# Kernel tuning notes

Hardware: AMD Instinct MI355X
Metric: run time of the kernel (lower is better)

Reference implementation:

```python
import jax, jax.numpy as jnp
import numpy as np

CUTOFF = 3  # cutoff_freq default in low_pass_filter


def _low_pass(x):
    # full 2D FFT over (H, W), keep only the 4 corner blocks of size CUTOFF
    H, W = x.shape[-2], x.shape[-1]
    f = jnp.fft.fftn(x, axes=(-2, -1))
    mask = jnp.zeros((H, W), dtype=x.dtype)
    c = CUTOFF
    mask = mask.at[:c, :c].set(1).at[:c, -c:].set(1).at[-c:, :c].set(1).at[-c:, -c:].set(1)
    return jnp.abs(jnp.fft.ifftn(f * mask, axes=(-2, -1)))


def setup_inputs() -> dict:
    key = jax.random.key(0)
    k_x, k_w1, k_b1, k_w2, k_b2 = jax.random.split(key, 5)
    n_feat = 8
    B, C, H, W = 32, 3, 512, 512
    x = jax.random.uniform(k_x, (B, C, H, W), dtype=jnp.float32)
    # 1x1 convs == channel-mixing matrices; kaiming-ish scale
    w1 = jax.random.normal(k_w1, (n_feat, C), dtype=jnp.float32) * (1.0 / np.sqrt(C))
    b1 = jax.random.normal(k_b1, (n_feat,), dtype=jnp.float32) * 0.01
    w2 = jax.random.normal(k_w2, (C, n_feat), dtype=jnp.float32) * (1.0 / np.sqrt(n_feat))
    b2 = jax.random.normal(k_b2, (C,), dtype=jnp.float32) * 0.01
    return {"x": x, "w1": w1, "b1": b1, "w2": w2, "b2": b2}


def reference(x, w1, b1, w2, b2):
    lp = _low_pass(x)                                        # [B,3,H,W]
    h = jax.nn.relu(jnp.einsum('bchw,fc->bfhw', lp, w1) + b1[None, :, None, None])
    y = jnp.einsum('bfhw,cf->bchw', h, w2) + b2[None, :, None, None]
    return jnp.clip(y + lp, 0.0, 1.0)
```

## Files before the change

kernel.cpp:

```cpp
#include <hip/hip_runtime.h>
#include <math.h>


#define WS_TS 0
#define WS_F  6144
#define WS_A  12288
constexpr int NPART = 8;

__global__ __launch_bounds__(512, 6) void k_colsum(const float* __restrict__ x,
                                                   float* __restrict__ ws) {
    __shared__ float buf[3][128][29];
    float* A = ws + WS_A;
    int img = blockIdx.x >> 3;
    int slab = blockIdx.x & 7;
    int t = threadIdx.x;
    int wq = t & 127;
    int q = t >> 7;
    int h0 = slab * 64 + q * 16;
    const float* xp = x + (size_t)img * 262144 + (size_t)h0 * 512 + wq * 4;

    const float TH = 6.28318530717958647692f / 512.0f;
    float pc1, ps1, pc2, ps2, pc3, ps3;
    sincosf(TH * (float)h0, &ps1, &pc1);
    pc2 = pc1 * pc1 - ps1 * ps1;  ps2 = 2.f * pc1 * ps1;
    pc3 = pc1 * pc2 - ps1 * ps2;  ps3 = ps1 * pc2 + pc1 * ps2;
    const float C1 = 0.99992470183914450299f, S1 = 0.01227153828571992539f;
    const float C2 = 0.99969881869620422012f, S2 = 0.02454122852291228803f;
    const float C3 = 0.99932238458834954375f, S3 = 0.03680722294135883171f;

    float s0[4] = {0,0,0,0};
    float ar1[4] = {0,0,0,0}, ai1[4] = {0,0,0,0};
    float ar2[4] = {0,0,0,0}, ai2[4] = {0,0,0,0};
    float ar3[4] = {0,0,0,0}, ai3[4] = {0,0,0,0};

    float4 cur[4], nxt[4];
#pragma unroll
    for (int j = 0; j < 4; ++j) cur[j] = *(const float4*)(xp + (size_t)j * 512);
#pragma unroll
    for (int g = 0; g < 4; ++g) {
        if (g < 3) {
#pragma unroll
            for (int j = 0; j < 4; ++j)
                nxt[j] = *(const float4*)(xp + (size_t)((g + 1) * 4 + j) * 512);
        }
#pragma unroll
        for (int j = 0; j < 4; ++j) {
            float xa[4] = {cur[j].x, cur[j].y, cur[j].z, cur[j].w};
#pragma unroll
            for (int u = 0; u < 4; ++u) {
                s0[u] += xa[u];
                ar1[u] = fmaf(xa[u], pc1, ar1[u]);  ai1[u] = fmaf(-xa[u], ps1, ai1[u]);
                ar2[u] = fmaf(xa[u], pc2, ar2[u]);  ai2[u] = fmaf(-xa[u], ps2, ai2[u]);
                ar3[u] = fmaf(xa[u], pc3, ar3[u]);  ai3[u] = fmaf(-xa[u], ps3, ai3[u]);
            }
            float n;
            n = pc1 * C1 - ps1 * S1;  ps1 = ps1 * C1 + pc1 * S1;  pc1 = n;
            n = pc2 * C2 - ps2 * S2;  ps2 = ps2 * C2 + pc2 * S2;  pc2 = n;
            n = pc3 * C3 - ps3 * S3;  ps3 = ps3 * C3 + pc3 * S3;  pc3 = n;
        }
#pragma unroll
        for (int j = 0; j < 4; ++j) cur[j] = nxt[j];
    }

    if (q != 0) {
        float* r = &buf[q - 1][wq][0];
#pragma unroll
        for (int u = 0; u < 4; ++u) {
            r[u]      = s0[u];
            r[4 + u]  = ar1[u];  r[8 + u]  = ai1[u];
            r[12 + u] = ar2[u];  r[16 + u] = ai2[u];
            r[20 + u] = ar3[u];  r[24 + u] = ai3[u];
        }
    }
    __syncthreads();
    if (q == 0) {
#pragma unroll
        for (int v = 0; v < 3; ++v) {
            const float* r = &buf[v][wq][0];
#pragma unroll
            for (int u = 0; u < 4; ++u) {
                s0[u]  += r[u];
                ar1[u] += r[4 + u];   ai1[u] += r[8 + u];
                ar2[u] += r[12 + u];  ai2[u] += r[16 + u];
                ar3[u] += r[20 + u];  ai3[u] += r[24 + u];
            }
        }
        float* Ab = A + (((size_t)img * NPART + slab) * 8) * 512 + wq * 4;
        *(float4*)(Ab + 0 * 512) = make_float4(s0[0], s0[1], s0[2], s0[3]);
        *(float4*)(Ab + 1 * 512) = make_float4(0.f, 0.f, 0.f, 0.f);
        *(float4*)(Ab + 2 * 512) = make_float4(ar1[0], ar1[1], ar1[2], ar1[3]);
        *(float4*)(Ab + 3 * 512) = make_float4(ai1[0], ai1[1], ai1[2], ai1[3]);
        *(float4*)(Ab + 4 * 512) = make_float4(ar2[0], ar2[1], ar2[2], ar2[3]);
        *(float4*)(Ab + 5 * 512) = make_float4(ai2[0], ai2[1], ai2[2], ai2[3]);
        *(float4*)(Ab + 6 * 512) = make_float4(ar3[0], ar3[1], ar3[2], ar3[3]);
        *(float4*)(Ab + 7 * 512) = make_float4(ai3[0], ai3[1], ai3[2], ai3[3]);
    }
}

__global__ __launch_bounds__(256) void k_proj(float* __restrict__ ws) {
    int t = threadIdx.x;
    if (blockIdx.x == 96) {
        const float STEP = 6.28318530717958647692f / 512.0f;
        const int mv[6] = {0, 1, 2, -3, -2, -1};
        for (int h = t; h < 512; h += 256) {
            float* tsp = ws + WS_TS + h * 12;
#pragma unroll
            for (int i = 0; i < 6; ++i) {
                int r = ((mv[i] * h) % 512 + 512) & 511;
                float s, c;
                sincosf(STEP * (float)r, &s, &c);
                tsp[2 * i] = c; tsp[2 * i + 1] = s;
            }
        }
        return;
    }
    __shared__ float As[8][8][68];
    __shared__ float Rs[28][8][2];
    const float* A = ws + WS_A;
    float* F = ws + WS_F;
    int img = blockIdx.x;

    {
        int plane = t >> 5;
        int w0 = (t & 31) * 16;
        float4 acc[4];
#pragma unroll
        for (int u = 0; u < 4; ++u) acc[u] = make_float4(0.f, 0.f, 0.f, 0.f);
        const float* base = A + ((size_t)img * NPART * 8 + plane) * 512 + w0;
        for (int hg = 0; hg < NPART; ++hg) {
            const float* p = base + (size_t)hg * 8 * 512;
#pragma unroll
            for (int u = 0; u < 4; ++u) {
                float4 v = *(const float4*)(p + u * 4);
                acc[u].x += v.x; acc[u].y += v.y; acc[u].z += v.z; acc[u].w += v.w;
            }
        }
        int seg = w0 >> 6, j0 = w0 & 63;
#pragma unroll
        for (int u = 0; u < 4; ++u)
            *(float4*)&As[plane][seg][j0 + u * 4] = acc[u];
    }
    __syncthreads();

    if (t < 224) {
        int pair = t >> 3, seg = t & 7;
        int k = pair / 7, mi = pair % 7;
        float m = (float)(mi - 3);
        const float TH = 6.28318530717958647692f / 512.0f;
        float cm, sm, pc, ps;
        sincosf(-m * TH, &sm, &cm);
        sincosf(-m * TH * (float)(seg * 64), &ps, &pc);
        const float* Ar_ = &As[2 * k][seg][0];
        const float* Ai_ = &As[2 * k + 1][seg][0];
        float pre = 0.f, pim = 0.f;
#pragma unroll 4
        for (int j = 0; j < 64; ++j) {
            float Ar = Ar_[j], Ai = Ai_[j];
            pre += Ar * pc - Ai * ps;
            pim += Ar * ps + Ai * pc;
            float n = pc * cm - ps * sm;
            ps = ps * cm + pc * sm;
            pc = n;
        }
        Rs[pair][seg][0] = pre;
        Rs[pair][seg][1] = pim;
    }
    __syncthreads();
    if (t < 56) {
        int pair = t >> 1, part = t & 1;
        float s = 0.f;
#pragma unroll
        for (int g = 0; g < 8; ++g) s += Rs[pair][g][part];
        F[(size_t)img * 56 + t] = s;
    }
}

__global__ __launch_bounds__(256) void k_out(const float* __restrict__ ws,
                                             const float* __restrict__ w1,
                                             const float* __restrict__ b1,
                                             const float* __restrict__ w2,
                                             const float* __restrict__ b2,
                                             float* __restrict__ out) {
    const float* tabS = ws + WS_TS;
    const float* Fb = ws + WS_F;
    __shared__ float F_lds[3][56];
    __shared__ float T[4][3][12];
    int t = threadIdx.x;
    int blk = blockIdx.x;
    int b = blk >> 7;
    int h0 = (blk & 127) << 2;

    if (t < 168) {
        int c = t / 56, comp = t % 56;
        F_lds[c][comp] = Fb[(size_t)(b * 3 + c) * 56 + comp];
    }

    float rw1[8][3], rb1[8], rw2[3][8], rb2[3];
#pragma unroll
    for (int f_ = 0; f_ < 8; ++f_) {
        rb1[f_] = b1[f_];
#pragma unroll
        for (int c = 0; c < 3; ++c) rw1[f_][c] = w1[f_ * 3 + c];
    }
#pragma unroll
    for (int c = 0; c < 3; ++c) {
        rb2[c] = b2[c];
#pragma unroll
        for (int f_ = 0; f_ < 8; ++f_) rw2[c][f_] = w2[c * 8 + f_];
    }
    __syncthreads();

    if (t < 72) {
        int rl = t / 18, rem = t % 18;
        int c = rem / 6, kc = rem % 6;
        int h = h0 + rl;
        const float* th = tabS + h * 12;
        int m_kc = (kc < 3) ? kc : kc - 6;
        const float inv = 1.0f / (512.0f * 512.0f);
        float tre = 0.f, tim = 0.f;
#pragma unroll
        for (int kr = 0; kr < 6; ++kr) {
            int kk, mi; float csign;
            if (kr < 3) { kk = kr;     mi = m_kc + 3; csign =  1.f; }
            else        { kk = 6 - kr; mi = 3 - m_kc; csign = -1.f; }
            int pair = kk * 7 + mi;
            float fr = F_lds[c][pair * 2] * inv;
            float fi = F_lds[c][pair * 2 + 1] * csign * inv;
            float cc = th[kr * 2], ss = th[kr * 2 + 1];
            tre += fr * cc - fi * ss;
            tim += fr * ss + fi * cc;
        }
        T[rl][c][kc * 2]     = tre;
        T[rl][c][kc * 2 + 1] = tim;
    }
    __syncthreads();

    int rl = t >> 6, lane = t & 63;
    int h = h0 + rl;
    float A0r[3], A0i[3], U1r[3], U1i[3], V1r[3], V1i[3];
    float U2r[3], U2i[3], V2r[3], V2i[3], Br[3], Bi[3];
#pragma unroll
    for (int c = 0; c < 3; ++c) {
        const float* Tc = T[rl][c];
        A0r[c] = Tc[0];  A0i[c] = Tc[1];
        float t1r = Tc[2],  t1i = Tc[3];
        float t2r = Tc[4],  t2i = Tc[5];
        float bmr = Tc[6],  bmi = Tc[7];
        float m2r = Tc[8],  m2i = Tc[9];
        float m1r = Tc[10], m1i = Tc[11];
        U1r[c] = t1r + m1r; U1i[c] = t1i + m1i;
        V1r[c] = t1r - m1r; V1i[c] = t1i - m1i;
        U2r[c] = t2r + m2r; U2i[c] = t2i + m2i;
        V2r[c] = t2r - m2r; V2i[c] = t2i - m2i;
        Br[c] = bmr; Bi[c] = bmi;
    }
    const float* tw = tabS + lane * 12;
    float c1 = tw[2], s1 = tw[3];
    float c2 = tw[4], s2 = tw[5];
    float c3 = tw[6], s3 = -tw[7];
    const float K = 0.70710678118654752440f;
    float* ob = out + ((size_t)(b * 3) * 512 + h) * 512;

#pragma unroll
    for (int j = 0; j < 8; ++j) {
        int w = lane + 64 * j;
        float lp[3];
#pragma unroll
        for (int c = 0; c < 3; ++c) {
            float re = A0r[c] + U1r[c] * c1 - V1i[c] * s1
                              + U2r[c] * c2 - V2i[c] * s2
                              + Br[c] * c3 + Bi[c] * s3;
            float im = A0i[c] + U1i[c] * c1 + V1r[c] * s1
                              + U2i[c] * c2 + V2r[c] * s2
                              + Bi[c] * c3 - Br[c] * s3;
            lp[c] = sqrtf(re * re + im * im);
        }
        float hid[8];
#pragma unroll
        for (int f_ = 0; f_ < 8; ++f_) {
            float v = rb1[f_] + lp[0] * rw1[f_][0] + lp[1] * rw1[f_][1] + lp[2] * rw1[f_][2];
            hid[f_] = fmaxf(v, 0.0f);
        }
#pragma unroll
        for (int c = 0; c < 3; ++c) {
            float y = rb2[c] + lp[c];
#pragma unroll
            for (int f_ = 0; f_ < 8; ++f_) y += hid[f_] * rw2[c][f_];
            y = fminf(fmaxf(y, 0.0f), 1.0f);
            ob[(size_t)c * 262144 + w] = y;
        }
        if (j < 7) {
            float nc1 = K * (c1 - s1), ns1 = K * (c1 + s1);
            float nc2 = -s2,           ns2 = c2;
            float nc3 = -K * (c3 + s3), ns3 = K * (c3 - s3);
            c1 = nc1; s1 = ns1; c2 = nc2; s2 = ns2; c3 = nc3; s3 = ns3;
        }
    }
}

extern "C" void kernel_launch(void* const* d_in, const int* in_sizes, int n_in,
                              void* d_out, int out_size, void* d_ws, size_t ws_size,
                              hipStream_t stream) {
    const float* x  = (const float*)d_in[0];
    const float* w1 = (const float*)d_in[1];
    const float* b1 = (const float*)d_in[2];
    const float* w2 = (const float*)d_in[3];
    const float* b2 = (const float*)d_in[4];
    float* out = (float*)d_out;
    float* ws = (float*)d_ws;

    hipLaunchKernelGGL(k_colsum, dim3(96 * NPART), dim3(512), 0, stream, x, ws);
    hipLaunchKernelGGL(k_proj, dim3(97), dim3(256), 0, stream, ws);
    hipLaunchKernelGGL(k_out, dim3(4096), dim3(256), 0, stream, ws, w1, b1, w2, b2, out);
}
```

Before: 69.74 us.

## Fold half-period row symmetry into column DFT and re-split colsum grid

The column-DFT kernel now loads rows h and h+256 together and uses their sum for even frequencies and their difference for odd frequencies. This halves the FMA work per loaded element. Twiddles come from compile-time per-row constants rather than a serial recurrence. The grid is re-split into 3072 blocks of 256 threads, each covering 8 row pairs over a 128-column stripe with float2 loads. The risk is that the narrower float2 accesses and the extra block count cost more than the arithmetic saved, since the kernel is likely memory-bound.

After: 66.51 us. 1.05x faster.

```diff
diff --git a/kernel.cpp b/kernel.cpp
--- a/kernel.cpp
+++ b/kernel.cpp
@@ -7,93 +7,106 @@
 #define WS_A  12288
 constexpr int NPART = 8;
 
-__global__ __launch_bounds__(512, 6) void k_colsum(const float* __restrict__ x,
+#define CJ0 1.0f
+#define CJ1 0.99992470183914450299f
+#define CJ2 0.99969881869620422012f
+#define CJ3 0.99932238458834954375f
+#define CJ4 0.99879545620517239271f
+#define CJ5 0.99811811290014917919f
+#define CJ6 0.99729045667869021614f
+#define CJ7 0.99631261218277800129f
+#define SJ0 0.0f
+#define SJ1 0.01227153828571992539f
+#define SJ2 0.02454122852291228803f
+#define SJ3 0.03680722294135883171f
+#define SJ4 0.04906767432741801425f
+#define SJ5 0.06132073630220857829f
+#define SJ6 0.07356456359966742631f
+#define SJ7 0.08579731234443989385f
+
+__global__ __launch_bounds__(256, 6) void k_colsum(const float* __restrict__ x,
                                                    float* __restrict__ ws) {
-    __shared__ float buf[3][128][29];
+    __shared__ float buf[3][64][15];
     float* A = ws + WS_A;
-    int img = blockIdx.x >> 3;
-    int slab = blockIdx.x & 7;
+    int img = blockIdx.x >> 5;
+    int sub = blockIdx.x & 31;
+    int stripe = sub & 3;
+    int hgrp = sub >> 2;
     int t = threadIdx.x;
-    int wq = t & 127;
-    int q = t >> 7;
-    int h0 = slab * 64 + q * 16;
-    const float* xp = x + (size_t)img * 262144 + (size_t)h0 * 512 + wq * 4;
+    int wave = t >> 6;
+    int lane = t & 63;
+    int w = stripe * 128 + lane * 2;
+    int H = hgrp * 32 + wave * 8;
+    const float* xp = x + (size_t)img * 262144 + (size_t)H * 512 + w;
 
     const float TH = 6.28318530717958647692f / 512.0f;
     float pc1, ps1, pc2, ps2, pc3, ps3;
-    sincosf(TH * (float)h0, &ps1, &pc1);
+    sincosf(TH * (float)H, &ps1, &pc1);
     pc2 = pc1 * pc1 - ps1 * ps1;  ps2 = 2.f * pc1 * ps1;
     pc3 = pc1 * pc2 - ps1 * ps2;  ps3 = ps1 * pc2 + pc1 * ps2;
-    const float C1 = 0.99992470183914450299f, S1 = 0.01227153828571992539f;
-    const float C2 = 0.99969881869620422012f, S2 = 0.02454122852291228803f;
-    const float C3 = 0.99932238458834954375f, S3 = 0.03680722294135883171f;
-
-    float s0[4] = {0,0,0,0};
-    float ar1[4] = {0,0,0,0}, ai1[4] = {0,0,0,0};
-    float ar2[4] = {0,0,0,0}, ai2[4] = {0,0,0,0};
-    float ar3[4] = {0,0,0,0}, ai3[4] = {0,0,0,0};
-
-    float4 cur[4], nxt[4];
-#pragma unroll
-    for (int j = 0; j < 4; ++j) cur[j] = *(const float4*)(xp + (size_t)j * 512);
-#pragma unroll
-    for (int g = 0; g < 4; ++g) {
-        if (g < 3) {
-#pragma unroll
-            for (int j = 0; j < 4; ++j)
-                nxt[j] = *(const float4*)(xp + (size_t)((g + 1) * 4 + j) * 512);
-        }
-#pragma unroll
-        for (int j = 0; j < 4; ++j) {
-            float xa[4] = {cur[j].x, cur[j].y, cur[j].z, cur[j].w};
-#pragma unroll
-            for (int u = 0; u < 4; ++u) {
-                s0[u] += xa[u];
-                ar1[u] = fmaf(xa[u], pc1, ar1[u]);  ai1[u] = fmaf(-xa[u], ps1, ai1[u]);
-                ar2[u] = fmaf(xa[u], pc2, ar2[u]);  ai2[u] = fmaf(-xa[u], ps2, ai2[u]);
-                ar3[u] = fmaf(xa[u], pc3, ar3[u]);  ai3[u] = fmaf(-xa[u], ps3, ai3[u]);
-            }
-            float n;
-            n = pc1 * C1 - ps1 * S1;  ps1 = ps1 * C1 + pc1 * S1;  pc1 = n;
-            n = pc2 * C2 - ps2 * S2;  ps2 = ps2 * C2 + pc2 * S2;  pc2 = n;
-            n = pc3 * C3 - ps3 * S3;  ps3 = ps3 * C3 + pc3 * S3;  pc3 = n;
-        }
-#pragma unroll
-        for (int j = 0; j < 4; ++j) cur[j] = nxt[j];
-    }
-
-    if (q != 0) {
-        float* r = &buf[q - 1][wq][0];
-#pragma unroll
-        for (int u = 0; u < 4; ++u) {
-            r[u]      = s0[u];
-            r[4 + u]  = ar1[u];  r[8 + u]  = ai1[u];
-            r[12 + u] = ar2[u];  r[16 + u] = ai2[u];
-            r[20 + u] = ar3[u];  r[24 + u] = ai3[u];
-        }
-    }
-    __syncthreads();
-    if (q == 0) {
+
+    float s0[2] = {0, 0};
+    float ar1[2] = {0, 0}, ai1[2] = {0, 0};
+    float ar2[2] = {0, 0}, ai2[2] = {0, 0};
+    float ar3[2] = {0, 0}, ai3[2] = {0, 0};
+
+#define ROW(J, CJ, SJ)                                                        \
+    {                                                                         \
+        float2 xa = *(const float2*)(xp + (size_t)(J) * 512);                 \
+        float2 xb = *(const float2*)(xp + (size_t)((J) * 512 + 131072));      \
+        float u0 = xa.x + xb.x, u1 = xa.y + xb.y;                             \
+        float v0 = xa.x - xb.x, v1 = xa.y - xb.y;                             \
+        float cj1 = pc1 * (CJ) - ps1 * (SJ);                                  \
+        float sj1 = ps1 * (CJ) + pc1 * (SJ);                                  \
+        float cj2 = cj1 * cj1 - sj1 * sj1;                                    \
+        float sj2 = 2.f * cj1 * sj1;                                          \
+        float cj3 = cj1 * cj2 - sj1 * sj2;                                    \
+        float sj3 = sj1 * cj2 + cj1 * sj2;                                    \
+        s0[0] += u0;               s0[1] += u1;                               \
+        ar1[0] = fmaf(v0, cj1, ar1[0]);  ai1[0] = fmaf(-v0, sj1, ai1[0]);     \
+        ar1[1] = fmaf(v1, cj1, ar1[1]);  ai1[1] = fmaf(-v1, sj1, ai1[1]);     \
+        ar2[0] = fmaf(u0, cj2, ar2[0]);  ai2[0] = fmaf(-u0, sj2, ai2[0]);     \
+        ar2[1] = fmaf(u1, cj2, ar2[1]);  ai2[1] = fmaf(-u1, sj2, ai2[1]);     \
+        ar3[0] = fmaf(v0, cj3, ar3[0]);  ai3[0] = fmaf(-v0, sj3, ai3[0]);     \
+        ar3[1] = fmaf(v1, cj3, ar3[1]);  ai3[1] = fmaf(-v1, sj3, ai3[1]);     \
+    }
+
+    ROW(0, CJ0, SJ0)
+    ROW(1, CJ1, SJ1)
+    ROW(2, CJ2, SJ2)
+    ROW(3, CJ3, SJ3)
+    ROW(4, CJ4, SJ4)
+    ROW(5, CJ5, SJ5)
+    ROW(6, CJ6, SJ6)
+    ROW(7, CJ7, SJ7)
+#undef ROW
+
+    if (wave != 0) {
+        float* r = &buf[wave - 1][lane][0];
+        r[0] = s0[0];   r[1] = s0[1];
+        r[2] = ar1[0];  r[3] = ar1[1];  r[4] = ai1[0];  r[5] = ai1[1];
+        r[6] = ar2[0];  r[7] = ar2[1];  r[8] = ai2[0];  r[9] = ai2[1];
+        r[10] = ar3[0]; r[11] = ar3[1]; r[12] = ai3[0]; r[13] = ai3[1];
+    }
+    __syncthreads();
+    if (wave == 0) {
 #pragma unroll
         for (int v = 0; v < 3; ++v) {
-            const float* r = &buf[v][wq][0];
-#pragma unroll
-            for (int u = 0; u < 4; ++u) {
-                s0[u]  += r[u];
-                ar1[u] += r[4 + u];   ai1[u] += r[8 + u];
-                ar2[u] += r[12 + u];  ai2[u] += r[16 + u];
-                ar3[u] += r[20 + u];  ai3[u] += r[24 + u];
-            }
-        }
-        float* Ab = A + (((size_t)img * NPART + slab) * 8) * 512 + wq * 4;
-        *(float4*)(Ab + 0 * 512) = make_float4(s0[0], s0[1], s0[2], s0[3]);
-        *(float4*)(Ab + 1 * 512) = make_float4(0.f, 0.f, 0.f, 0.f);
-        *(float4*)(Ab + 2 * 512) = make_float4(ar1[0], ar1[1], ar1[2], ar1[3]);
-        *(float4*)(Ab + 3 * 512) = make_float4(ai1[0], ai1[1], ai1[2], ai1[3]);
-        *(float4*)(Ab + 4 * 512) = make_float4(ar2[0], ar2[1], ar2[2], ar2[3]);
-        *(float4*)(Ab + 5 * 512) = make_float4(ai2[0], ai2[1], ai2[2], ai2[3]);
-        *(float4*)(Ab + 6 * 512) = make_float4(ar3[0], ar3[1], ar3[2], ar3[3]);
-        *(float4*)(Ab + 7 * 512) = make_float4(ai3[0], ai3[1], ai3[2], ai3[3]);
+            const float* r = &buf[v][lane][0];
+            s0[0] += r[0];   s0[1] += r[1];
+            ar1[0] += r[2];  ar1[1] += r[3];  ai1[0] += r[4];  ai1[1] += r[5];
+            ar2[0] += r[6];  ar2[1] += r[7];  ai2[0] += r[8];  ai2[1] += r[9];
+            ar3[0] += r[10]; ar3[1] += r[11]; ai3[0] += r[12]; ai3[1] += r[13];
+        }
+        float* Ab = A + (((size_t)img * NPART + hgrp) * 8) * 512 + w;
+        *(float2*)(Ab + 0 * 512) = make_float2(s0[0], s0[1]);
+        *(float2*)(Ab + 1 * 512) = make_float2(0.f, 0.f);
+        *(float2*)(Ab + 2 * 512) = make_float2(ar1[0], ar1[1]);
+        *(float2*)(Ab + 3 * 512) = make_float2(ai1[0], ai1[1]);
+        *(float2*)(Ab + 4 * 512) = make_float2(ar2[0], ar2[1]);
+        *(float2*)(Ab + 5 * 512) = make_float2(ai2[0], ai2[1]);
+        *(float2*)(Ab + 6 * 512) = make_float2(ar3[0], ar3[1]);
+        *(float2*)(Ab + 7 * 512) = make_float2(ai3[0], ai3[1]);
     }
 }
 
@@ -309,7 +322,7 @@
     float* out = (float*)d_out;
     float* ws = (float*)d_ws;
 
-    hipLaunchKernelGGL(k_colsum, dim3(96 * NPART), dim3(512), 0, stream, x, ws);
+    hipLaunchKernelGGL(k_colsum, dim3(96 * 32), dim3(256), 0, stream, x, ws);
     hipLaunchKernelGGL(k_proj, dim3(97), dim3(256), 0, stream, ws);
     hipLaunchKernelGGL(k_out, dim3(4096), dim3(256), 0, stream, ws, w1, b1, w2, b2, out);
 }
```
